# Kernel tuning notes

Hardware: AMD Instinct MI355X
Metric: run time of the kernel (lower is better)

The kernel has to match this reference:

```python
import jax, jax.numpy as jnp
import numpy as np

N_NODES = 100000
N_EDGES = 1600000
D_FEAT = 64


def setup_inputs() -> dict:
    key = jax.random.key(0)
    k1, k2, k3 = jax.random.split(key, 3)
    x = jax.random.normal(k1, (N_NODES, D_FEAT), dtype=jnp.float32)
    edge_index = jax.random.randint(k2, (2, N_EDGES), 0, N_NODES, dtype=jnp.int64)
    edge_attr = jax.random.uniform(k3, (N_EDGES,), dtype=jnp.float32)
    return {"x": x, "edge_index": edge_index, "edge_attr": edge_attr}


def reference(x, edge_index, edge_attr):
    # out[row[i]] += exp(-edge_attr[i]) * x[col[i]]  for every edge i
    row, col = edge_index[0], edge_index[1]
    B = jnp.exp(-edge_attr)                      # [E] per-edge scalar kernel
    msgs = B[:, None] * x[col]                   # [E, D] gather + scale
    out = jax.ops.segment_sum(msgs, row, num_segments=N_NODES)  # scatter-add
    return out
```

## Files before the change

### kernel.cpp

```cpp
#include <hip/hip_runtime.h>
#include <math.h>

#define N_NODES_C 100000
#define D_FEAT 64

#define CB_SHIFT 8
#define CB_SIZE 256
#define NCB ((N_NODES_C + CB_SIZE - 1) / CB_SIZE)
#define CAP_E 8192
#define COL_BITS 17
#define COL_MASK17 0x1FFFF
#define CHUNK 4096

__global__ void spline_scatter_atomic(const float* __restrict__ x,
                                      const int* __restrict__ row_idx,
                                      const int* __restrict__ col_idx,
                                      const float* __restrict__ edge_attr,
                                      float* __restrict__ out,
                                      int n_edges) {
    long long t = (long long)blockIdx.x * blockDim.x + threadIdx.x;
    int e = (int)(t >> 6);
    int f = (int)(t & 63);
    if (e >= n_edges) return;
    int r = row_idx[e];
    int c = col_idx[e];
    float w = expf(-edge_attr[e]);
    atomicAdd(&out[(long long)r * D_FEAT + f], w * x[(long long)c * D_FEAT + f]);
}


__global__ void hist_kernel(const int* __restrict__ row_idx, int* __restrict__ counts,
                            int n_edges) {
    int e = blockIdx.x * blockDim.x + threadIdx.x;
    if (e < n_edges) atomicAdd(&counts[row_idx[e]], 1);
}

__global__ void scan_kernel(const int* __restrict__ counts, int* __restrict__ start,
                            int* __restrict__ cursor, int n) {
    __shared__ int wave_sums[16];
    __shared__ int carry_s;
    const int tid = threadIdx.x;
    const int lane = tid & 63;
    const int wid = tid >> 6;
    if (tid == 0) carry_s = 0;
    __syncthreads();
    for (int base = 0; base < n; base += 1024) {
        int i = base + tid;
        int v = (i < n) ? counts[i] : 0;
        int inc = v;
        #pragma unroll
        for (int d = 1; d < 64; d <<= 1) {
            int t = __shfl_up(inc, d, 64);
            if (lane >= d) inc += t;
        }
        if (lane == 63) wave_sums[wid] = inc;
        __syncthreads();
        if (tid == 0) {
            int s = carry_s;
            #pragma unroll
            for (int k = 0; k < 16; ++k) { int t = wave_sums[k]; wave_sums[k] = s; s += t; }
            carry_s = s;
        }
        __syncthreads();
        int excl = inc - v + wave_sums[wid];
        if (i < n) { start[i] = excl; cursor[i] = excl; }
        __syncthreads();
    }
    if (tid == 0) start[n] = carry_s;
}

__global__ void bucket_kernel(const int* __restrict__ row_idx,
                              const int* __restrict__ col_idx,
                              const float* __restrict__ edge_attr,
                              int* __restrict__ cursor,
                              int2* __restrict__ colw,
                              int n_edges) {
    int e = blockIdx.x * blockDim.x + threadIdx.x;
    if (e >= n_edges) return;
    int r = row_idx[e];
    int c = col_idx[e];
    float w = expf(-edge_attr[e]);
    int pos = atomicAdd(&cursor[r], 1);
    colw[pos] = make_int2(c, __float_as_int(w));
}

__global__ void gather_accum_kernel(const float* __restrict__ x,
                                    const int* __restrict__ start,
                                    const int2* __restrict__ colw,
                                    float* __restrict__ out,
                                    int n_nodes) {
    int node = blockIdx.x * (blockDim.x >> 6) + (threadIdx.x >> 6);
    int lane = threadIdx.x & 63;
    if (node >= n_nodes) return;
    int b = start[node];
    int e = start[node + 1];
    float acc = 0.0f;
    int j = b;
    for (; j + 3 < e; j += 4) {
        int2 c0 = colw[j], c1 = colw[j + 1], c2 = colw[j + 2], c3 = colw[j + 3];
        float x0 = x[(size_t)c0.x * D_FEAT + lane];
        float x1 = x[(size_t)c1.x * D_FEAT + lane];
        float x2 = x[(size_t)c2.x * D_FEAT + lane];
        float x3 = x[(size_t)c3.x * D_FEAT + lane];
        acc += __int_as_float(c0.y) * x0;
        acc += __int_as_float(c1.y) * x1;
        acc += __int_as_float(c2.y) * x2;
        acc += __int_as_float(c3.y) * x3;
    }
    for (; j < e; ++j) {
        int2 c0 = colw[j];
        acc += __int_as_float(c0.y) * x[(size_t)c0.x * D_FEAT + lane];
    }
    out[(size_t)node * D_FEAT + lane] = acc;
}


__global__ void init_cursor_kernel(int* __restrict__ ccursor) {
    int i = blockIdx.x * blockDim.x + threadIdx.x;
    if (i < NCB) ccursor[i] = i * CAP_E;
}

__global__ __launch_bounds__(256) void agg_scatter_kernel(const int* __restrict__ row,
                                                          const int* __restrict__ col,
                                                          const float* __restrict__ attr,
                                                          int* __restrict__ ccursor,
                                                          int2* __restrict__ cw,
                                                          int n_edges) {
    __shared__ int h[NCB];
    __shared__ int gbase[NCB];
    __shared__ int lcur[NCB];
    const int tid = threadIdx.x;
    const int base = blockIdx.x * CHUNK;
    for (int i = tid; i < NCB; i += 256) { h[i] = 0; lcur[i] = 0; }
    __syncthreads();
    #pragma unroll
    for (int k = 0; k < CHUNK / 256; ++k) {
        int e = base + k * 256 + tid;
        if (e < n_edges) atomicAdd(&h[row[e] >> CB_SHIFT], 1);
    }
    __syncthreads();
    for (int i = tid; i < NCB; i += 256) {
        int c = h[i];
        gbase[i] = c ? atomicAdd(&ccursor[i], c) : 0;
    }
    __syncthreads();
    #pragma unroll
    for (int k = 0; k < CHUNK / 256; ++k) {
        int e = base + k * 256 + tid;
        if (e < n_edges) {
            int r = row[e];
            int b = r >> CB_SHIFT;
            float w = expf(-attr[e]);
            int p = gbase[b] + atomicAdd(&lcur[b], 1);
            if (p < (b + 1) * CAP_E)
                cw[p] = make_int2(col[e] | ((r & (CB_SIZE - 1)) << COL_BITS),
                                  __float_as_int(w));
        }
    }
}

__global__ __launch_bounds__(1024) void bucket_fused_kernel(const float* __restrict__ x,
                                                            const int2* __restrict__ cw,
                                                            const int* __restrict__ ccursor,
                                                            float* __restrict__ out,
                                                            int n_nodes) {
    __shared__ int2 sorted[CAP_E];
    __shared__ int lhist[CB_SIZE];
    __shared__ int lbase[CB_SIZE];
    __shared__ int lcur[CB_SIZE];
    __shared__ int wsum[4];
    const int b = blockIdx.x;
    const int tid = threadIdx.x;
    const int lane = tid & 63;
    const int wid = tid >> 6;
    const int beg = b * CAP_E;
    int end = ccursor[b];
    if (end > beg + CAP_E) end = beg + CAP_E;
    const int n = end - beg;

    if (tid < CB_SIZE) lhist[tid] = 0;
    __syncthreads();

    int2 my[CAP_E / 1024];
    #pragma unroll
    for (int k = 0; k < CAP_E / 1024; ++k) {
        int i = tid + k * 1024;
        if (i < n) {
            int2 d = cw[beg + i];
            my[k] = d;
            atomicAdd(&lhist[(d.x >> COL_BITS) & (CB_SIZE - 1)], 1);
        }
    }
    __syncthreads();

    int v = 0, inc = 0;
    if (tid < CB_SIZE) {
        v = lhist[tid];
        inc = v;
        #pragma unroll
        for (int d = 1; d < 64; d <<= 1) {
            int t = __shfl_up(inc, d, 64);
            if (lane >= d) inc += t;
        }
        if (lane == 63) wsum[wid] = inc;
    }
    __syncthreads();
    if (tid == 0) {
        int s = 0;
        #pragma unroll
        for (int k = 0; k < 4; ++k) { int t = wsum[k]; wsum[k] = s; s += t; }
    }
    __syncthreads();
    if (tid < CB_SIZE) {
        int excl = inc - v + wsum[wid];
        lbase[tid] = excl;
        lcur[tid] = excl;
    }
    __syncthreads();

    #pragma unroll
    for (int k = 0; k < CAP_E / 1024; ++k) {
        int i = tid + k * 1024;
        if (i < n) {
            int2 d = my[k];
            int ln = (d.x >> COL_BITS) & (CB_SIZE - 1);
            int p = atomicAdd(&lcur[ln], 1);
            sorted[p] = make_int2(d.x & COL_MASK17, d.y);
        }
    }
    __syncthreads();

    const int node0 = b * CB_SIZE;
    for (int t2 = 0; t2 < 16; ++t2) {
        int ln = wid * 16 + t2;
        int node = node0 + ln;
        if (node >= n_nodes) break;
        int s = lbase[ln];
        int e2 = (ln + 1 < CB_SIZE) ? lbase[ln + 1] : n;
        float acc = 0.0f;
        int j = s;
        for (; j + 8 <= e2; j += 8) {
            #pragma unroll
            for (int k = 0; k < 8; ++k) {
                int2 d = sorted[j + k];
                acc += __int_as_float(d.y) * x[(size_t)d.x * D_FEAT + lane];
            }
        }
        {
            int rem = e2 - j;
            #pragma unroll
            for (int k = 0; k < 7; ++k) {
                if (k < rem) {
                    int2 d = sorted[j + k];
                    acc += __int_as_float(d.y) * x[(size_t)d.x * D_FEAT + lane];
                }
            }
        }
        out[(size_t)node * D_FEAT + lane] = acc;
    }
}

extern "C" void kernel_launch(void* const* d_in, const int* in_sizes, int n_in,
                              void* d_out, int out_size, void* d_ws, size_t ws_size,
                              hipStream_t stream) {
    const float* x    = (const float*)d_in[0];
    const int*   eidx = (const int*)d_in[1];
    const float* attr = (const float*)d_in[2];
    float*       out  = (float*)d_out;

    const int n_edges = in_sizes[2];
    const int n_nodes = N_NODES_C;
    const int* row = eidx;
    const int* col = eidx + n_edges;

    size_t off_cw   = 0;
    size_t off_ccur = off_cw + (size_t)NCB * CAP_E * sizeof(int2);
    size_t ws_needed_new = off_ccur + (size_t)NCB * sizeof(int);

    const double mean_fill = (double)n_edges / (double)NCB;
    const bool cap_ok = mean_fill + 12.0 * sqrt(mean_fill) + 256.0 <= (double)CAP_E;

    if (ws_size >= ws_needed_new && cap_ok) {
        char* ws = (char*)d_ws;
        int2* cw      = (int2*)(ws + off_cw);
        int*  ccursor = (int*)(ws + off_ccur);

        init_cursor_kernel<<<(NCB + 255) / 256, 256, 0, stream>>>(ccursor);
        const int cb = (n_edges + CHUNK - 1) / CHUNK;
        agg_scatter_kernel<<<cb, 256, 0, stream>>>(row, col, attr, ccursor, cw, n_edges);
        bucket_fused_kernel<<<NCB, 1024, 0, stream>>>(x, cw, ccursor, out, n_nodes);
        return;
    }

    size_t l_off_colw   = 0;
    size_t l_off_counts = l_off_colw + (size_t)n_edges * sizeof(int2);
    size_t l_off_start  = l_off_counts + (size_t)n_nodes * sizeof(int);
    size_t l_off_cursor = l_off_start + (size_t)(n_nodes + 1) * sizeof(int);
    size_t ws_needed_old = l_off_cursor + (size_t)n_nodes * sizeof(int);

    if (ws_size >= ws_needed_old) {
        char* ws = (char*)d_ws;
        int2* colw   = (int2*)(ws + l_off_colw);
        int*  counts = (int*)(ws + l_off_counts);
        int*  start  = (int*)(ws + l_off_start);
        int*  cursor = (int*)(ws + l_off_cursor);

        hipMemsetAsync(counts, 0, (size_t)n_nodes * sizeof(int), stream);

        const int eb = (n_edges + 255) / 256;
        hist_kernel<<<eb, 256, 0, stream>>>(row, counts, n_edges);
        scan_kernel<<<1, 1024, 0, stream>>>(counts, start, cursor, n_nodes);
        bucket_kernel<<<eb, 256, 0, stream>>>(row, col, attr, cursor, colw, n_edges);

        const int waves_per_block = 4;
        const int nb = (n_nodes + waves_per_block - 1) / waves_per_block;
        gather_accum_kernel<<<nb, 256, 0, stream>>>(x, start, colw, out, n_nodes);
        return;
    }

    hipMemsetAsync(out, 0, (size_t)out_size * sizeof(float), stream);
    const long long total = (long long)n_edges * 64;
    const int blocks = (int)((total + 255) / 256);
    spline_scatter_atomic<<<blocks, 256, 0, stream>>>(x, row, col, attr, out, n_edges);
}
```

Measured before the change: 172.8 us.

## Interleave row buckets modulo 512 and resize aggregation grid for balanced load

```diff
diff --git a/kernel.cpp b/kernel.cpp
--- a/kernel.cpp
+++ b/kernel.cpp
@@ -4,13 +4,15 @@
 #define N_NODES_C 100000
 #define D_FEAT 64
 
-#define CB_SHIFT 8
-#define CB_SIZE 256
-#define NCB ((N_NODES_C + CB_SIZE - 1) / CB_SIZE)
-#define CAP_E 8192
+#define NB_F 512
+#define FB_SHIFT 9
+#define FB_MASK (NB_F - 1)
+#define LMAX 256
+#define CAP_E 4096
 #define COL_BITS 17
 #define COL_MASK17 0x1FFFF
-#define CHUNK 4096
+#define NB_AGG 512
+#define AGG_ITERS 8
 
 __global__ void spline_scatter_atomic(const float* __restrict__ x,
                                       const int* __restrict__ row_idx,
@@ -98,14 +100,10 @@
     int j = b;
     for (; j + 3 < e; j += 4) {
         int2 c0 = colw[j], c1 = colw[j + 1], c2 = colw[j + 2], c3 = colw[j + 3];
-        float x0 = x[(size_t)c0.x * D_FEAT + lane];
-        float x1 = x[(size_t)c1.x * D_FEAT + lane];
-        float x2 = x[(size_t)c2.x * D_FEAT + lane];
-        float x3 = x[(size_t)c3.x * D_FEAT + lane];
-        acc += __int_as_float(c0.y) * x0;
-        acc += __int_as_float(c1.y) * x1;
-        acc += __int_as_float(c2.y) * x2;
-        acc += __int_as_float(c3.y) * x3;
+        acc += __int_as_float(c0.y) * x[(size_t)c0.x * D_FEAT + lane];
+        acc += __int_as_float(c1.y) * x[(size_t)c1.x * D_FEAT + lane];
+        acc += __int_as_float(c2.y) * x[(size_t)c2.x * D_FEAT + lane];
+        acc += __int_as_float(c3.y) * x[(size_t)c3.x * D_FEAT + lane];
     }
     for (; j < e; ++j) {
         int2 c0 = colw[j];
@@ -117,57 +115,61 @@
 
 __global__ void init_cursor_kernel(int* __restrict__ ccursor) {
     int i = blockIdx.x * blockDim.x + threadIdx.x;
-    if (i < NCB) ccursor[i] = i * CAP_E;
-}
-
-__global__ __launch_bounds__(256) void agg_scatter_kernel(const int* __restrict__ row,
-                                                          const int* __restrict__ col,
-                                                          const float* __restrict__ attr,
-                                                          int* __restrict__ ccursor,
-                                                          int2* __restrict__ cw,
-                                                          int n_edges) {
-    __shared__ int h[NCB];
-    __shared__ int gbase[NCB];
-    __shared__ int lcur[NCB];
+    if (i < NB_F) ccursor[i] = i * CAP_E;
+}
+
+__global__ __launch_bounds__(512) void agg_scatter2_kernel(const int* __restrict__ row,
+                                                           const int* __restrict__ col,
+                                                           const float* __restrict__ attr,
+                                                           int* __restrict__ ccursor,
+                                                           int2* __restrict__ cw,
+                                                           int n_edges, int chunk) {
+    __shared__ int h[NB_F];
+    __shared__ int gbase[NB_F];
+    __shared__ int lcur[NB_F];
     const int tid = threadIdx.x;
-    const int base = blockIdx.x * CHUNK;
-    for (int i = tid; i < NCB; i += 256) { h[i] = 0; lcur[i] = 0; }
-    __syncthreads();
+    const int base = blockIdx.x * chunk;
+    const int end = min(base + chunk, n_edges);
+    h[tid] = 0;
+    lcur[tid] = 0;
+    __syncthreads();
+    int rc[AGG_ITERS];
     #pragma unroll
-    for (int k = 0; k < CHUNK / 256; ++k) {
-        int e = base + k * 256 + tid;
-        if (e < n_edges) atomicAdd(&h[row[e] >> CB_SHIFT], 1);
-    }
-    __syncthreads();
-    for (int i = tid; i < NCB; i += 256) {
-        int c = h[i];
-        gbase[i] = c ? atomicAdd(&ccursor[i], c) : 0;
+    for (int k = 0; k < AGG_ITERS; ++k) {
+        int e = base + k * 512 + tid;
+        rc[k] = (e < end) ? row[e] : -1;
+        if (rc[k] >= 0) atomicAdd(&h[rc[k] & FB_MASK], 1);
+    }
+    __syncthreads();
+    {
+        int c = h[tid];
+        gbase[tid] = c ? atomicAdd(&ccursor[tid], c) : 0;
     }
     __syncthreads();
     #pragma unroll
-    for (int k = 0; k < CHUNK / 256; ++k) {
-        int e = base + k * 256 + tid;
-        if (e < n_edges) {
-            int r = row[e];
-            int b = r >> CB_SHIFT;
+    for (int k = 0; k < AGG_ITERS; ++k) {
+        int e = base + k * 512 + tid;
+        int r = rc[k];
+        if (r >= 0) {
+            int b = r & FB_MASK;
             float w = expf(-attr[e]);
             int p = gbase[b] + atomicAdd(&lcur[b], 1);
             if (p < (b + 1) * CAP_E)
-                cw[p] = make_int2(col[e] | ((r & (CB_SIZE - 1)) << COL_BITS),
+                cw[p] = make_int2(col[e] | ((r >> FB_SHIFT) << COL_BITS),
                                   __float_as_int(w));
         }
     }
 }
 
-__global__ __launch_bounds__(1024) void bucket_fused_kernel(const float* __restrict__ x,
-                                                            const int2* __restrict__ cw,
-                                                            const int* __restrict__ ccursor,
-                                                            float* __restrict__ out,
-                                                            int n_nodes) {
+__global__ __launch_bounds__(1024) void bucket_fused2_kernel(const float* __restrict__ x,
+                                                             const int2* __restrict__ cw,
+                                                             const int* __restrict__ ccursor,
+                                                             float* __restrict__ out,
+                                                             int n_nodes) {
     __shared__ int2 sorted[CAP_E];
-    __shared__ int lhist[CB_SIZE];
-    __shared__ int lbase[CB_SIZE];
-    __shared__ int lcur[CB_SIZE];
+    __shared__ int lhist[LMAX];
+    __shared__ int lbase[LMAX];
+    __shared__ int lcur[LMAX];
     __shared__ int wsum[4];
     const int b = blockIdx.x;
     const int tid = threadIdx.x;
@@ -178,7 +180,7 @@
     if (end > beg + CAP_E) end = beg + CAP_E;
     const int n = end - beg;
 
-    if (tid < CB_SIZE) lhist[tid] = 0;
+    if (tid < LMAX) lhist[tid] = 0;
     __syncthreads();
 
     int2 my[CAP_E / 1024];
@@ -188,13 +190,13 @@
         if (i < n) {
             int2 d = cw[beg + i];
             my[k] = d;
-            atomicAdd(&lhist[(d.x >> COL_BITS) & (CB_SIZE - 1)], 1);
+            atomicAdd(&lhist[d.x >> COL_BITS], 1);
         }
     }
     __syncthreads();
 
     int v = 0, inc = 0;
-    if (tid < CB_SIZE) {
+    if (tid < LMAX) {
         v = lhist[tid];
         inc = v;
         #pragma unroll
@@ -211,7 +213,7 @@
         for (int k = 0; k < 4; ++k) { int t = wsum[k]; wsum[k] = s; s += t; }
     }
     __syncthreads();
-    if (tid < CB_SIZE) {
+    if (tid < LMAX) {
         int excl = inc - v + wsum[wid];
         lbase[tid] = excl;
         lcur[tid] = excl;
@@ -223,20 +225,19 @@
         int i = tid + k * 1024;
         if (i < n) {
             int2 d = my[k];
-            int ln = (d.x >> COL_BITS) & (CB_SIZE - 1);
+            int ln = d.x >> COL_BITS;
             int p = atomicAdd(&lcur[ln], 1);
             sorted[p] = make_int2(d.x & COL_MASK17, d.y);
         }
     }
     __syncthreads();
 
-    const int node0 = b * CB_SIZE;
     for (int t2 = 0; t2 < 16; ++t2) {
-        int ln = wid * 16 + t2;
-        int node = node0 + ln;
+        int ln = t2 * 16 + wid;
+        int node = b + (ln << FB_SHIFT);
         if (node >= n_nodes) break;
         int s = lbase[ln];
-        int e2 = (ln + 1 < CB_SIZE) ? lbase[ln + 1] : n;
+        int e2 = (ln + 1 < LMAX) ? lbase[ln + 1] : n;
         float acc = 0.0f;
         int j = s;
         for (; j + 8 <= e2; j += 8) {
@@ -274,21 +275,24 @@
     const int* col = eidx + n_edges;
 
     size_t off_cw   = 0;
-    size_t off_ccur = off_cw + (size_t)NCB * CAP_E * sizeof(int2);
-    size_t ws_needed_new = off_ccur + (size_t)NCB * sizeof(int);
-
-    const double mean_fill = (double)n_edges / (double)NCB;
-    const bool cap_ok = mean_fill + 12.0 * sqrt(mean_fill) + 256.0 <= (double)CAP_E;
+    size_t off_ccur = off_cw + (size_t)NB_F * CAP_E * sizeof(int2);
+    size_t ws_needed_new = off_ccur + (size_t)NB_F * sizeof(int);
+
+    const int chunk = (n_edges + NB_AGG - 1) / NB_AGG;
+    const double mean_fill = (double)n_edges / (double)NB_F;
+    bool cap_ok = (mean_fill + 12.0 * sqrt(mean_fill) + 128.0) <= (double)CAP_E;
+    cap_ok = cap_ok && (chunk <= 512 * AGG_ITERS);
+    cap_ok = cap_ok && (n_nodes <= NB_F * LMAX);
 
     if (ws_size >= ws_needed_new && cap_ok) {
         char* ws = (char*)d_ws;
         int2* cw      = (int2*)(ws + off_cw);
         int*  ccursor = (int*)(ws + off_ccur);
 
-        init_cursor_kernel<<<(NCB + 255) / 256, 256, 0, stream>>>(ccursor);
-        const int cb = (n_edges + CHUNK - 1) / CHUNK;
-        agg_scatter_kernel<<<cb, 256, 0, stream>>>(row, col, attr, ccursor, cw, n_edges);
-        bucket_fused_kernel<<<NCB, 1024, 0, stream>>>(x, cw, ccursor, out, n_nodes);
+        init_cursor_kernel<<<(NB_F + 255) / 256, 256, 0, stream>>>(ccursor);
+        agg_scatter2_kernel<<<NB_AGG, 512, 0, stream>>>(row, col, attr, ccursor, cw,
+                                                        n_edges, chunk);
+        bucket_fused2_kernel<<<NB_F, 1024, 0, stream>>>(x, cw, ccursor, out, n_nodes);
         return;
     }
 
```

After: 164.0 us. -5.1%, faster.
